# Kernel tuning notes

Measured on AMD Instinct MI355X. Metric: run time of the kernel, lower is better.

The kernel has to match this reference:

```python
import jax, jax.numpy as jnp
import numpy as np

N_LAYERS = 11
DILATIONS = tuple(2 ** i for i in range(N_LAYERS))   # 1..1024
MEM_SIZES = DILATIONS                                 # kernel=2 -> 1 past tap -> mem = dilation
HOP = 128
C_SCALE = 1.0
FFT = 256       # channel width
NUM_CLS = 256   # mu-law classes
COND = 80       # mel bands
FRAMES = 16


def setup_inputs() -> dict:
    key = jax.random.key(0)
    ks = jax.random.split(key, 10)
    s = 0.05  # keep logits well-scaled for softmax sampling
    return {
        "y": jax.random.normal(ks[0], (COND, FRAMES), jnp.float32),
        "samples": jax.random.uniform(ks[1], (FRAMES * HOP,), jnp.float32),
        "emb_raw": jax.random.normal(ks[2], (NUM_CLS, FFT), jnp.float32) * 0.5,
        "condition_W": jax.random.normal(ks[3], (N_LAYERS * FFT, COND), jnp.float32) * s,
        "WV_past": jax.random.normal(ks[4], (N_LAYERS, FFT, FFT, 1), jnp.float32) * s,
        "WV_present": jax.random.normal(ks[5], (N_LAYERS, FFT, FFT), jnp.float32) * s,
        "W_o_w": jax.random.normal(ks[6], (N_LAYERS, FFT, FFT), jnp.float32) * s,
        "W_o_b": jax.random.normal(ks[7], (N_LAYERS, FFT), jnp.float32) * s,
        "end_w": jax.random.normal(ks[8], (NUM_CLS, FFT), jnp.float32) * s,
        "end_b": jax.random.normal(ks[9], (NUM_CLS,), jnp.float32) * s,
    }


def reference(y, samples, emb_raw, condition_W, WV_past, WV_present, W_o_w, W_o_b, end_w, end_b):
    emb = jnp.tanh(emb_raw)                      # fftnet.emb[0].weight.tanh()
    T = y.shape[1] * HOP
    # F.interpolate nearest with scale_factor=hop_length == frame repeat
    yu = jnp.repeat(y, HOP, axis=1)              # [COND, T]
    # precompute all conditioning projections (condition_W @ y[:, i], chunked per layer)
    conds = (condition_W @ yu).reshape(N_LAYERS, FFT, T).transpose(2, 0, 1)  # [T, L, FFT]

    bufs0 = tuple(jnp.zeros((FFT, m), jnp.float32) for m in MEM_SIZES)
    x0 = emb[NUM_CLS // 2 - 1]
    n_taps = WV_past.shape[3]

    def step(carry, inp):
        x, bufs = carry
        cond_t, u, t = inp
        new_bufs = []
        for j in range(N_LAYERS):
            mem = bufs[j]
            m = MEM_SIZES[j]
            idx = t % m                                   # ring-buffer write/oldest-read ptr
            h = cond_t[j]
            ii = idx
            for k in range(n_taps):                       # read past taps (before write)
                h = h + WV_past[j, :, :, k] @ mem[:, ii]
                ii = (ii + DILATIONS[j]) % m
            h = h + WV_present[j] @ x
            new_bufs.append(mem.at[:, idx].set(x))        # write current x into ring buffer
            h = jax.nn.relu(h)
            z = W_o_w[j] @ h + W_o_b[j]
            x = jax.nn.relu(z + x)                        # residual + relu
        logits = (end_w @ x + end_b) * C_SCALE
        cum = jnp.cumsum(jax.nn.softmax(logits))
        new_idx = jnp.argmax(cum > u)                     # nonzero(cum > u)[0]
        return (emb[new_idx], tuple(new_bufs)), new_idx

    ts = jnp.arange(T)
    _, outputs = jax.lax.scan(step, (x0, bufs0), (conds, samples, ts))
    return outputs  # [T] int sampled mu-law classes
```

## Files before the change

kernel.cpp:

```cpp
#include <hip/hip_runtime.h>
#include <math.h>


#define T_STEPS 2048
#define NBLK    33

#define OFF_EMBT   0
#define OFF_WPET   65536
#define OFF_WVPET  131072
#define OFF_RINGS  196608
#define OFF_TAPS   1244672
#define OFF_Z      1285632
#define OFF_H0     1291264
#define WS_FLOATS  1291520

#define FZ(j,s)  ((((j)*2)+(s))*32)
#define FTAP(j)  ((21+(j))*32)
#define FH0      (32*32)
#define FBAR(b)  ((40+(b))*32)
#define NZERO_INTS  1280
#define NFLAG_INTS  4096

__device__ __forceinline__ float ldc(const float* p) {
  int v = __hip_atomic_load((const int*)p, __ATOMIC_RELAXED, __HIP_MEMORY_SCOPE_AGENT);
  return __int_as_float(v);
}
__device__ __forceinline__ void stc(float* p, float x) {
  __hip_atomic_store((int*)p, __float_as_int(x), __ATOMIC_RELAXED, __HIP_MEMORY_SCOPE_AGENT);
}
__device__ __forceinline__ void wait1(int* f, int want) {
  int it = 0;
  while (__hip_atomic_load(f, __ATOMIC_RELAXED, __HIP_MEMORY_SCOPE_AGENT) < want) {
    if (++it > (1 << 24)) break;
  }
  (void)__hip_atomic_load(f, __ATOMIC_ACQUIRE, __HIP_MEMORY_SCOPE_AGENT);
}
__device__ __forceinline__ void post(int* f, int v) {
  __hip_atomic_store(f, v, __ATOMIC_RELEASE, __HIP_MEMORY_SCOPE_AGENT);
}

__global__ __launch_bounds__(512)
void fftnet_kernel(const float* __restrict__ y, const float* __restrict__ samples,
                   const float* __restrict__ emb_raw, const float* __restrict__ condW,
                   const float* __restrict__ WV_past, const float* __restrict__ WV_present,
                   const float* __restrict__ W_o_w, const float* __restrict__ W_o_b,
                   const float* __restrict__ end_w, const float* __restrict__ end_b,
                   int* __restrict__ out, float* __restrict__ ws)
{
  const int tid = threadIdx.x;
  const int bid = blockIdx.x;
  int* iflags = (int*)(ws + WS_FLOATS);

  __shared__ float s_x[256];
  __shared__ float s_h[256];
  __shared__ float s_p[1024];
  __shared__ float s_cond[16 * 256];
  __shared__ float s_m[320];
  __shared__ unsigned long long s_mask[8];
  __shared__ int s_i[16];

  if (bid == 0) {
    for (int i = tid; i < NZERO_INTS; i += 512)
      __hip_atomic_store(iflags + i, 0, __ATOMIC_RELAXED, __HIP_MEMORY_SCOPE_AGENT);
  }
  for (int i = bid * 512 + tid; i < 65536; i += NBLK * 512)
    stc(ws + OFF_EMBT + i, tanhf(emb_raw[i]));

  __syncthreads();
  if (tid == 0) post(iflags + FBAR(bid), 1);
  if (tid < NBLK) wait1(iflags + FBAR(tid), 1);
  __syncthreads();

  for (int n = bid; n < 512; n += NBLK) {
    const float* wmat = (n < 256) ? WV_present : WV_past;
    int cls = n & 255;
    int c = tid & 255, s2 = tid >> 8;
    float acc = 0.f;
    for (int k = 128 * s2; k < 128 * s2 + 128; ++k)
      acc += wmat[c * 256 + k] * ws[OFF_EMBT + cls * 256 + k];
    s_p[s2 * 256 + c] = acc;
    __syncthreads();
    if (tid < 256)
      stc(ws + ((n < 256) ? OFF_WPET : OFF_WVPET) + cls * 256 + tid, s_p[tid] + s_p[256 + tid]);
    __syncthreads();
  }

  __syncthreads();
  if (tid == 0) post(iflags + FBAR(bid), 2);
  if (tid < NBLK) wait1(iflags + FBAR(tid), 2);
  __syncthreads();

  if (bid == 0) {
    const int c = tid & 255, s2 = tid >> 8;
    float we[128];
#pragma unroll
    for (int i = 0; i < 128; ++i) we[i] = end_w[c * 256 + 128 * s2 + i];
    const float eb = end_b[c];
    const float b10 = W_o_b[10 * 256 + c];
    for (int e = tid; e < 4096; e += 512) {
      int f = e >> 8, r = e & 255;
      float a = 0.f;
      for (int q = 0; q < 80; ++q) a += condW[r * 80 + q] * y[q * 16 + f];
      s_cond[f * 256 + r] = a;
    }
    __syncthreads();
    float* h0 = ws + OFF_H0;
    float* ring0 = ws + OFF_RINGS;
    float* zA = ws + OFF_Z + (10 * 2 + 0) * 256;
    float* zB = ws + OFF_Z + (10 * 2 + 1) * 256;
    float* ring10 = ws + OFF_RINGS + 512 * 1023;
    if (tid < 256) {
      float hv = s_cond[tid] + ws[OFF_WPET + 127 * 256 + tid];
      stc(h0 + tid, fmaxf(hv, 0.f));
      stc(ring0 + tid, ws[OFF_EMBT + 127 * 256 + tid]);
    }
    __syncthreads();
    if (tid == 0) post(iflags + FH0, 1);
    int pidx = 127;
    const int lane = tid & 63, w = tid >> 6;

    for (int t = 0; t < T_STEPS; ++t) {
      float qv = (tid < 256) ? ws[OFF_WVPET + pidx * 256 + tid] : 0.f;
      if (tid < 2) wait1(iflags + FZ(10, tid), t + 1);
      __syncthreads();
      if (tid < 256) {
        float xo = ldc(zA + tid) + ldc(zB + tid) + b10 + ldc(ring10 + (t & 2047) * 256 + tid);
        s_x[tid] = fmaxf(xo, 0.f);
      }
      __syncthreads();
      float acc = 0.f;
#pragma unroll
      for (int i = 0; i < 128; ++i) acc += we[i] * s_x[128 * s2 + i];
      s_p[s2 * 256 + c] = acc;
      __syncthreads();
      float logit = 0.f;
      if (tid < 256) logit = s_p[tid] + s_p[256 + tid] + eb;
      float vmax = (tid < 256) ? logit : -3.4e38f;
#pragma unroll
      for (int d = 32; d > 0; d >>= 1) vmax = fmaxf(vmax, __shfl_xor(vmax, d, 64));
      if (lane == 0) s_m[280 + w] = vmax;
      __syncthreads();
      float mx = fmaxf(fmaxf(s_m[280], s_m[281]), fmaxf(s_m[282], s_m[283]));
      float e = (tid < 256) ? expf(logit - mx) : 0.f;
      float vs = e;
#pragma unroll
      for (int d = 32; d > 0; d >>= 1) vs += __shfl_xor(vs, d, 64);
      if (lane == 0) s_m[288 + w] = vs;
      __syncthreads();
      float ssum = s_m[288] + s_m[289] + s_m[290] + s_m[291];
      float u = samples[t];
      float p = (tid < 256) ? (e / ssum) : 0.f;
      float v = p;
#pragma unroll
      for (int d = 1; d < 64; d <<= 1) {
        float o = __shfl_up(v, (unsigned)d, 64);
        if (lane >= d) v += o;
      }
      if (tid < 256 && lane == 63) s_m[256 + w] = v;
      __syncthreads();
      float offs = 0.f;
      if (tid < 256) for (int k = 0; k < w; ++k) offs += s_m[256 + k];
      float cum = v + offs;
      unsigned long long msk = __ballot(tid < 256 && (cum > u));
      if (lane == 0) s_mask[w] = msk;
      __syncthreads();
      if (tid == 0) {
        int idx = 0;
        for (int k = 0; k < 4; ++k) {
          unsigned long long m2 = s_mask[k];
          if (m2) { idx = k * 64 + (int)__builtin_ctzll(m2); break; }
        }
        s_i[0] = idx;
        out[t] = idx;
      }
      __syncthreads();
      int idx = s_i[0];
      if (t + 1 < T_STEPS) {
        int f1 = (t + 1) >> 7;
        if (tid < 256) {
          float hv = s_cond[f1 * 256 + tid] + ws[OFF_WPET + idx * 256 + tid] + qv;
          stc(h0 + tid, fmaxf(hv, 0.f));
          stc(ring0 + ((t + 1) & 1) * 256 + tid, ws[OFF_EMBT + idx * 256 + tid]);
        }
        __syncthreads();
        if (tid == 0) post(iflags + FH0, t + 2);
      }
      pidx = idx;
    }

  } else if (bid <= 22) {
    int j, side;
    if (bid <= 10)      { j = bid;      side = 0; }
    else if (bid <= 20) { j = bid - 10; side = 1; }
    else                { j = 0;        side = bid - 21; }
    const int base = side * 128;
    float wo[64];
    {
      const float* W = W_o_w + j * 65536;
      int c = tid & 255, s2 = tid >> 8;
#pragma unroll
      for (int i = 0; i < 64; ++i) wo[i] = W[c * 256 + base + 64 * s2 + i];
    }

    if (j == 0) {
      float* h0 = ws + OFF_H0;
      float* zout = ws + OFF_Z + side * 256;
      const int c = tid & 255, s2 = tid >> 8;
      for (int t = 0; t < T_STEPS; ++t) {
        if (tid == 0) wait1(iflags + FH0, t + 1);
        __syncthreads();
        if (tid < 128) s_h[tid] = ldc(h0 + base + tid);
        __syncthreads();
        float acc = 0.f;
#pragma unroll
        for (int i = 0; i < 64; ++i) acc += wo[i] * s_h[64 * s2 + i];
        s_p[s2 * 256 + c] = acc;
        __syncthreads();
        if (tid < 256) stc(zout + tid, s_p[tid] + s_p[256 + tid]);
        __syncthreads();
        if (tid == 0) post(iflags + FZ(0, side), t + 1);
      }
    } else {
      float wp[64];
      {
        const float* W = WV_present + j * 65536;
        int r = tid & 127, s = tid >> 7;
#pragma unroll
        for (int i = 0; i < 64; ++i) wp[i] = W[(base + r) * 256 + 64 * s + i];
      }
      const float bprev = W_o_b[(j - 1) * 256 + (tid & 255)];
      for (int e = tid; e < 2048; e += 512) {
        int f = e >> 7, rr = e & 127;
        float a = 0.f;
        for (int q = 0; q < 80; ++q) a += condW[(j * 256 + base + rr) * 80 + q] * y[q * 16 + f];
        s_cond[f * 128 + rr] = a;
      }
      __syncthreads();
      const int dj = 1 << j, maskj = 2 * dj - 1;
      const int dprev = 1 << (j - 1), maskp = 2 * dprev - 1;
      float* ringp = ws + OFF_RINGS + 512 * (dprev - 1);
      float* ringj = ws + OFF_RINGS + 512 * (dj - 1);
      float* zpa = ws + OFF_Z + ((j - 1) * 2 + 0) * 256;
      float* zpb = ws + OFF_Z + ((j - 1) * 2 + 1) * 256;
      float* zout = ws + OFF_Z + (j * 2 + side) * 256;
      float* tapj = ws + OFF_TAPS + (j - 1) * 16 * 256;

      for (int t = 0; t < T_STEPS; ++t) {
        if (tid == 0) wait1(iflags + FTAP(j), t + 1);
        __syncthreads();
        float tv = (tid < 128) ? ldc(tapj + (t & 15) * 256 + base + tid) : 0.f;
        if (tid < 2) wait1(iflags + FZ(j - 1, tid), t + 1);
        __syncthreads();
        if (tid < 256) {
          float xv = ldc(zpa + tid) + ldc(zpb + tid) + bprev
                   + ldc(ringp + (t & maskp) * 256 + tid);
          xv = fmaxf(xv, 0.f);
          s_x[tid] = xv;
          if (side == 0) stc(ringj + (t & maskj) * 256 + tid, xv);
        }
        __syncthreads();
        {
          int r = tid & 127, s = tid >> 7;
          float acc = 0.f;
#pragma unroll
          for (int i = 0; i < 64; ++i) acc += wp[i] * s_x[64 * s + i];
          s_p[s * 128 + r] = acc;
        }
        __syncthreads();
        if (tid < 128) {
          int f = t >> 7;
          float hv = s_p[tid] + s_p[128 + tid] + s_p[256 + tid] + s_p[384 + tid]
                   + s_cond[f * 128 + tid] + tv;
          s_h[tid] = fmaxf(hv, 0.f);
        }
        __syncthreads();
        {
          int cc = tid & 255, s2 = tid >> 8;
          float acc = 0.f;
#pragma unroll
          for (int i = 0; i < 64; ++i) acc += wo[i] * s_h[64 * s2 + i];
          s_p[s2 * 256 + cc] = acc;
        }
        __syncthreads();
        if (tid < 256) stc(zout + tid, s_p[tid] + s_p[256 + tid]);
        __syncthreads();
        if (tid == 0) post(iflags + FZ(j, side), t + 1);
      }
    }

  } else {
    const int j = bid - 22;
    const int dj = 1 << j, maskj = 2 * dj - 1;
    float wq[128];
    {
      const float* W = WV_past + j * 65536;
      int r = tid & 255, s2 = tid >> 8;
#pragma unroll
      for (int i = 0; i < 128; ++i) wq[i] = W[r * 256 + 128 * s2 + i];
    }
    float* ringj = ws + OFF_RINGS + 512 * (dj - 1);
    float* tapj = ws + OFF_TAPS + (j - 1) * 16 * 256;
    const int lag = (dj < 16) ? dj : 16;

    for (int t = 0; t < T_STEPS; ++t) {
      int want = t - lag + 1;
      if (tid == 0 && want >= 1) wait1(iflags + FZ(j, 0), want);
      __syncthreads();
      if (t >= dj) {
        if (tid < 256) s_x[tid] = ldc(ringj + ((t - dj) & maskj) * 256 + tid);
        __syncthreads();
        int r = tid & 255, s2 = tid >> 8;
        float acc = 0.f;
#pragma unroll
        for (int i = 0; i < 128; ++i) acc += wq[i] * s_x[128 * s2 + i];
        s_p[s2 * 256 + r] = acc;
        __syncthreads();
        if (tid < 256) stc(tapj + (t & 15) * 256 + tid, s_p[tid] + s_p[256 + tid]);
      } else {
        if (tid < 256) stc(tapj + (t & 15) * 256 + tid, 0.f);
      }
      __syncthreads();
      if (tid == 0) post(iflags + FTAP(j), t + 1);
    }
  }
}

extern "C" void kernel_launch(void* const* d_in, const int* in_sizes, int n_in,
                              void* d_out, int out_size, void* d_ws, size_t ws_size,
                              hipStream_t stream) {
  const float* y       = (const float*)d_in[0];
  const float* samples = (const float*)d_in[1];
  const float* emb_raw = (const float*)d_in[2];
  const float* condW   = (const float*)d_in[3];
  const float* WV_past = (const float*)d_in[4];
  const float* WV_pres = (const float*)d_in[5];
  const float* W_o_w   = (const float*)d_in[6];
  const float* W_o_b   = (const float*)d_in[7];
  const float* end_w   = (const float*)d_in[8];
  const float* end_b   = (const float*)d_in[9];
  (void)in_sizes; (void)n_in; (void)out_size; (void)ws_size;
  hipLaunchKernelGGL(fftnet_kernel, dim3(NBLK), dim3(512), 0, stream,
                     y, samples, emb_raw, condW, WV_past, WV_pres,
                     W_o_w, W_o_b, end_w, end_b, (int*)d_out, (float*)d_ws);
}
```

Baseline: 59.14 ms.

## Pin pipeline roles to one XCC and use L2-coherent CAS loads for handoff

```diff
diff --git a/kernel.cpp b/kernel.cpp
--- a/kernel.cpp
+++ b/kernel.cpp
@@ -3,7 +3,8 @@
 
 
 #define T_STEPS 2048
-#define NBLK    33
+#define NROLE   32
+#define NBLK    256
 
 #define OFF_EMBT   0
 #define OFF_WPET   65536
@@ -11,27 +12,25 @@
 #define OFF_RINGS  196608
 #define OFF_TAPS   1244672
 #define OFF_Z      1285632
-#define OFF_H0     1291264
 #define WS_FLOATS  1291520
 
 #define FZ(j,s)  ((((j)*2)+(s))*32)
 #define FTAP(j)  ((21+(j))*32)
-#define FH0      (32*32)
-#define FBAR(b)  ((40+(b))*32)
-#define NZERO_INTS  1280
-#define NFLAG_INTS  4096
-
-__device__ __forceinline__ float ldc(const float* p) {
-  int v = __hip_atomic_load((const int*)p, __ATOMIC_RELAXED, __HIP_MEMORY_SCOPE_AGENT);
-  return __int_as_float(v);
-}
+#define FIDX     (32*32)
+#define FBAR(r)  ((40+(r))*32)
+#define NZERO_INTS 1280
+#define CHOSEN   2432
+#define TICKET   2464
+
+#define XCC_GETREG ((31 << 11) | 20)
+
 __device__ __forceinline__ void stc(float* p, float x) {
   __hip_atomic_store((int*)p, __float_as_int(x), __ATOMIC_RELAXED, __HIP_MEMORY_SCOPE_AGENT);
 }
 __device__ __forceinline__ void wait1(int* f, int want) {
   int it = 0;
   while (__hip_atomic_load(f, __ATOMIC_RELAXED, __HIP_MEMORY_SCOPE_AGENT) < want) {
-    if (++it > (1 << 24)) break;
+    if (++it > (1 << 22)) break;
   }
   (void)__hip_atomic_load(f, __ATOMIC_ACQUIRE, __HIP_MEMORY_SCOPE_AGENT);
 }
@@ -39,7 +38,28 @@
   __hip_atomic_store(f, v, __ATOMIC_RELEASE, __HIP_MEMORY_SCOPE_AGENT);
 }
 
-__global__ __launch_bounds__(512)
+#define SENT  0x7fffffff
+#define SENT2 0x7ffffffe
+__device__ __forceinline__ int ld_i32_l2(int* p) {
+  int e = SENT;
+  __hip_atomic_compare_exchange_strong(p, &e, SENT2, __ATOMIC_RELAXED,
+                                       __ATOMIC_RELAXED, __HIP_MEMORY_SCOPE_WORKGROUP);
+  return e;
+}
+__device__ __forceinline__ float ld_f32_l2(float* p) {
+  int e = SENT;
+  __hip_atomic_compare_exchange_strong((int*)p, &e, SENT2, __ATOMIC_RELAXED,
+                                       __ATOMIC_RELAXED, __HIP_MEMORY_SCOPE_WORKGROUP);
+  return __int_as_float(e);
+}
+__device__ __forceinline__ int wait_l2(int* f, int want, int& budget) {
+  int v;
+  do { v = ld_i32_l2(f); } while (v < want && --budget > 0);
+  return v;
+}
+__device__ __forceinline__ void drain() { asm volatile("s_waitcnt vmcnt(0)" ::: "memory"); }
+
+__global__ __launch_bounds__(512, 2)
 void fftnet_kernel(const float* __restrict__ y, const float* __restrict__ samples,
                    const float* __restrict__ emb_raw, const float* __restrict__ condW,
                    const float* __restrict__ WV_past, const float* __restrict__ WV_present,
@@ -48,7 +68,6 @@
                    int* __restrict__ out, float* __restrict__ ws)
 {
   const int tid = threadIdx.x;
-  const int bid = blockIdx.x;
   int* iflags = (int*)(ws + WS_FLOATS);
 
   __shared__ float s_x[256];
@@ -57,21 +76,46 @@
   __shared__ float s_cond[16 * 256];
   __shared__ float s_m[320];
   __shared__ unsigned long long s_mask[8];
-  __shared__ int s_i[16];
-
-  if (bid == 0) {
-    for (int i = tid; i < NZERO_INTS; i += 512)
-      __hip_atomic_store(iflags + i, 0, __ATOMIC_RELAXED, __HIP_MEMORY_SCOPE_AGENT);
-  }
-  for (int i = bid * 512 + tid; i < 65536; i += NBLK * 512)
+  __shared__ int s_i[2];
+
+  if (blockIdx.x == 0) {
+    for (int i = tid; i < NZERO_INTS; i += 512) iflags[i] = 0;
+    drain();
+    if (tid == 0)
+      __hip_atomic_store(iflags + TICKET, 0, __ATOMIC_RELAXED, __HIP_MEMORY_SCOPE_AGENT);
+    __threadfence();
+    __syncthreads();
+    if (tid == 0) {
+      int xcc = __builtin_amdgcn_s_getreg(XCC_GETREG) & 15;
+      __hip_atomic_store(iflags + CHOSEN, xcc + 1, __ATOMIC_RELEASE, __HIP_MEMORY_SCOPE_AGENT);
+    }
+  }
+  if (tid == 0) {
+    int ch, it = 0;
+    do {
+      ch = __hip_atomic_load(iflags + CHOSEN, __ATOMIC_ACQUIRE, __HIP_MEMORY_SCOPE_AGENT);
+    } while ((ch < 1 || ch > 16) && ++it < (1 << 24));
+    int xcc = __builtin_amdgcn_s_getreg(XCC_GETREG) & 15;
+    int role = -1;
+    if (xcc == ch - 1) {
+      int tk = __hip_atomic_fetch_add(iflags + TICKET, 1, __ATOMIC_RELAXED,
+                                      __HIP_MEMORY_SCOPE_AGENT);
+      if (tk < NROLE) role = tk;
+    }
+    s_i[0] = role;
+  }
+  __syncthreads();
+  const int role = s_i[0];
+  if (role < 0) return;
+
+  for (int i = role * 512 + tid; i < 65536; i += NROLE * 512)
     stc(ws + OFF_EMBT + i, tanhf(emb_raw[i]));
-
-  __syncthreads();
-  if (tid == 0) post(iflags + FBAR(bid), 1);
-  if (tid < NBLK) wait1(iflags + FBAR(tid), 1);
-  __syncthreads();
-
-  for (int n = bid; n < 512; n += NBLK) {
+  __syncthreads();
+  if (tid == 0) post(iflags + FBAR(role), 1);
+  if (tid < NROLE) wait1(iflags + FBAR(tid), 1);
+  __syncthreads();
+
+  for (int n = role; n < 512; n += NROLE) {
     const float* wmat = (n < 256) ? WV_present : WV_past;
     int cls = n & 255;
     int c = tid & 255, s2 = tid >> 8;
@@ -84,48 +128,37 @@
       stc(ws + ((n < 256) ? OFF_WPET : OFF_WVPET) + cls * 256 + tid, s_p[tid] + s_p[256 + tid]);
     __syncthreads();
   }
-
-  __syncthreads();
-  if (tid == 0) post(iflags + FBAR(bid), 2);
-  if (tid < NBLK) wait1(iflags + FBAR(tid), 2);
-  __syncthreads();
-
-  if (bid == 0) {
+  __syncthreads();
+  if (tid == 0) post(iflags + FBAR(role), 2);
+  if (tid < NROLE) wait1(iflags + FBAR(tid), 2);
+  __syncthreads();
+  __builtin_amdgcn_fence(__ATOMIC_ACQUIRE, "agent");
+  __syncthreads();
+
+  int budget = 1 << 22;
+
+  if (role == 0) {
     const int c = tid & 255, s2 = tid >> 8;
     float we[128];
 #pragma unroll
     for (int i = 0; i < 128; ++i) we[i] = end_w[c * 256 + 128 * s2 + i];
     const float eb = end_b[c];
     const float b10 = W_o_b[10 * 256 + c];
-    for (int e = tid; e < 4096; e += 512) {
-      int f = e >> 8, r = e & 255;
-      float a = 0.f;
-      for (int q = 0; q < 80; ++q) a += condW[r * 80 + q] * y[q * 16 + f];
-      s_cond[f * 256 + r] = a;
-    }
-    __syncthreads();
-    float* h0 = ws + OFF_H0;
-    float* ring0 = ws + OFF_RINGS;
     float* zA = ws + OFF_Z + (10 * 2 + 0) * 256;
     float* zB = ws + OFF_Z + (10 * 2 + 1) * 256;
     float* ring10 = ws + OFF_RINGS + 512 * 1023;
-    if (tid < 256) {
-      float hv = s_cond[tid] + ws[OFF_WPET + 127 * 256 + tid];
-      stc(h0 + tid, fmaxf(hv, 0.f));
-      stc(ring0 + tid, ws[OFF_EMBT + 127 * 256 + tid]);
-    }
-    __syncthreads();
-    if (tid == 0) post(iflags + FH0, 1);
-    int pidx = 127;
     const int lane = tid & 63, w = tid >> 6;
+    if (tid == 0) iflags[FIDX] = (1 << 8) | 127;
 
     for (int t = 0; t < T_STEPS; ++t) {
-      float qv = (tid < 256) ? ws[OFF_WVPET + pidx * 256 + tid] : 0.f;
-      if (tid < 2) wait1(iflags + FZ(10, tid), t + 1);
+      float u = samples[t];
+      if (tid < 2) wait_l2(iflags + FZ(10, 0) + tid * 32, t + 1, budget);
       __syncthreads();
       if (tid < 256) {
-        float xo = ldc(zA + tid) + ldc(zB + tid) + b10 + ldc(ring10 + (t & 2047) * 256 + tid);
-        s_x[tid] = fmaxf(xo, 0.f);
+        float a = ld_f32_l2(zA + tid);
+        float b = ld_f32_l2(zB + tid);
+        float r3 = ld_f32_l2(ring10 + (t & 2047) * 256 + tid);
+        s_x[tid] = fmaxf(a + b + b10 + r3, 0.f);
       }
       __syncthreads();
       float acc = 0.f;
@@ -148,7 +181,6 @@
       if (lane == 0) s_m[288 + w] = vs;
       __syncthreads();
       float ssum = s_m[288] + s_m[289] + s_m[290] + s_m[291];
-      float u = samples[t];
       float p = (tid < 256) ? (e / ssum) : 0.f;
       float v = p;
 #pragma unroll
@@ -170,144 +202,155 @@
           unsigned long long m2 = s_mask[k];
           if (m2) { idx = k * 64 + (int)__builtin_ctzll(m2); break; }
         }
-        s_i[0] = idx;
+        iflags[FIDX] = ((t + 2) << 8) | idx;
         out[t] = idx;
       }
       __syncthreads();
-      int idx = s_i[0];
-      if (t + 1 < T_STEPS) {
-        int f1 = (t + 1) >> 7;
-        if (tid < 256) {
-          float hv = s_cond[f1 * 256 + tid] + ws[OFF_WPET + idx * 256 + tid] + qv;
-          stc(h0 + tid, fmaxf(hv, 0.f));
-          stc(ring0 + ((t + 1) & 1) * 256 + tid, ws[OFF_EMBT + idx * 256 + tid]);
+    }
+
+  } else if (role == 1) {
+    float wo0[128];
+    { int c = tid & 255, s2 = tid >> 8;
+#pragma unroll
+      for (int i = 0; i < 128; ++i) wo0[i] = W_o_w[c * 256 + 128 * s2 + i]; }
+    const float b0 = W_o_b[tid & 255];
+    for (int e = tid; e < 4096; e += 512) {
+      int f = e >> 8, r = e & 255;
+      float a = 0.f;
+      for (int q = 0; q < 80; ++q) a += condW[r * 80 + q] * y[q * 16 + f];
+      s_cond[f * 256 + r] = a;
+    }
+    __syncthreads();
+    float* x1 = ws + OFF_Z;
+    int pidx = 127;
+
+    for (int t = 0; t < T_STEPS; ++t) {
+      float tapv = 0.f;
+      if (tid < 256 && t > 0) tapv = ws[OFF_WVPET + pidx * 256 + tid];
+      if (tid == 0) {
+        int v = wait_l2(iflags + FIDX, (t + 1) << 8, budget);
+        s_i[1] = v & 255;
+      }
+      __syncthreads();
+      const int idx = s_i[1];
+      if (tid < 256) {
+        s_x[tid] = ws[OFF_EMBT + idx * 256 + tid];
+        float hv = s_cond[(t >> 7) * 256 + tid] + ws[OFF_WPET + idx * 256 + tid] + tapv;
+        s_h[tid] = fmaxf(hv, 0.f);
+      }
+      __syncthreads();
+      {
+        int c = tid & 255, s2 = tid >> 8;
+        float a0 = 0.f, a1 = 0.f;
+#pragma unroll
+        for (int i = 0; i < 64; ++i) a0 += wo0[i] * s_h[128 * s2 + i];
+#pragma unroll
+        for (int i = 0; i < 64; ++i) a1 += wo0[64 + i] * s_h[128 * s2 + 64 + i];
+        s_p[s2 * 256 + c] = a0 + a1;
+      }
+      __syncthreads();
+      if (tid < 256)
+        x1[tid] = fmaxf(s_p[tid] + s_p[256 + tid] + b0 + s_x[tid], 0.f);
+      drain();
+      __syncthreads();
+      if (tid == 0) iflags[FZ(0, 0)] = t + 1;
+      pidx = idx;
+    }
+
+  } else if (role <= 21) {
+    const int jj = (role <= 11) ? (role - 1) : (role - 11);
+    const int side = (role <= 11) ? 0 : 1;
+    const int base = side * 128;
+    float wp[64], wo[64];
+    { const float* W = WV_present + jj * 65536;
+      int r = tid & 127, s = tid >> 7;
+#pragma unroll
+      for (int i = 0; i < 64; ++i) wp[i] = W[(base + r) * 256 + 64 * s + i]; }
+    { const float* W = W_o_w + jj * 65536;
+      int c = tid & 255, s2 = tid >> 8;
+#pragma unroll
+      for (int i = 0; i < 64; ++i) wo[i] = W[c * 256 + base + 64 * s2 + i]; }
+    const float bprev = W_o_b[(jj - 1) * 256 + (tid & 255)];
+    for (int e = tid; e < 2048; e += 512) {
+      int f = e >> 7, rr = e & 127;
+      float a = 0.f;
+      for (int q = 0; q < 80; ++q) a += condW[(jj * 256 + base + rr) * 80 + q] * y[q * 16 + f];
+      s_cond[f * 128 + rr] = a;
+    }
+    __syncthreads();
+    const int dj = 1 << jj, maskj = 2 * dj - 1;
+    const int dprev = 1 << (jj - 1), maskp = 2 * dprev - 1;
+    float* ringp = ws + OFF_RINGS + 512 * (dprev - 1);
+    float* ringj = ws + OFF_RINGS + 512 * (dj - 1);
+    float* zpa = ws + OFF_Z + ((jj - 1) * 2 + 0) * 256;
+    float* zpb = ws + OFF_Z + ((jj - 1) * 2 + 1) * 256;
+    float* zout = ws + OFF_Z + (jj * 2 + side) * 256;
+    float* tapj = ws + OFF_TAPS + (jj - 1) * 16 * 256;
+    const int nz = (jj == 1) ? 1 : 2;
+
+    for (int t = 0; t < T_STEPS; ++t) {
+      if (tid < nz) wait_l2(iflags + FZ(jj - 1, 0) + tid * 32, t + 1, budget);
+      if (tid == 2) wait_l2(iflags + FTAP(jj), t + 1, budget);
+      __syncthreads();
+      float tv = 0.f;
+      if (tid < 256) {
+        float xv;
+        if (jj == 1) {
+          xv = ld_f32_l2(zpa + tid);
+        } else {
+          float a = ld_f32_l2(zpa + tid);
+          float b = ld_f32_l2(zpb + tid);
+          float r3 = ld_f32_l2(ringp + (t & maskp) * 256 + tid);
+          xv = fmaxf(a + b + bprev + r3, 0.f);
         }
-        __syncthreads();
-        if (tid == 0) post(iflags + FH0, t + 2);
-      }
-      pidx = idx;
-    }
-
-  } else if (bid <= 22) {
-    int j, side;
-    if (bid <= 10)      { j = bid;      side = 0; }
-    else if (bid <= 20) { j = bid - 10; side = 1; }
-    else                { j = 0;        side = bid - 21; }
-    const int base = side * 128;
-    float wo[64];
-    {
-      const float* W = W_o_w + j * 65536;
-      int c = tid & 255, s2 = tid >> 8;
-#pragma unroll
-      for (int i = 0; i < 64; ++i) wo[i] = W[c * 256 + base + 64 * s2 + i];
-    }
-
-    if (j == 0) {
-      float* h0 = ws + OFF_H0;
-      float* zout = ws + OFF_Z + side * 256;
-      const int c = tid & 255, s2 = tid >> 8;
-      for (int t = 0; t < T_STEPS; ++t) {
-        if (tid == 0) wait1(iflags + FH0, t + 1);
-        __syncthreads();
-        if (tid < 128) s_h[tid] = ldc(h0 + base + tid);
-        __syncthreads();
+        s_x[tid] = xv;
+        if (side == 0) ringj[(t & maskj) * 256 + tid] = xv;
+      }
+      if (tid < 128) tv = ld_f32_l2(tapj + (t & 15) * 256 + base + tid);
+      __syncthreads();
+      { int r = tid & 127, s = tid >> 7;
         float acc = 0.f;
 #pragma unroll
+        for (int i = 0; i < 64; ++i) acc += wp[i] * s_x[64 * s + i];
+        s_p[s * 128 + r] = acc; }
+      __syncthreads();
+      if (tid < 128) {
+        int f = t >> 7;
+        float hv = s_p[tid] + s_p[128 + tid] + s_p[256 + tid] + s_p[384 + tid]
+                 + s_cond[f * 128 + tid] + tv;
+        s_h[tid] = fmaxf(hv, 0.f);
+      }
+      __syncthreads();
+      { int cc = tid & 255, s2 = tid >> 8;
+        float acc = 0.f;
+#pragma unroll
         for (int i = 0; i < 64; ++i) acc += wo[i] * s_h[64 * s2 + i];
-        s_p[s2 * 256 + c] = acc;
-        __syncthreads();
-        if (tid < 256) stc(zout + tid, s_p[tid] + s_p[256 + tid]);
-        __syncthreads();
-        if (tid == 0) post(iflags + FZ(0, side), t + 1);
-      }
-    } else {
-      float wp[64];
-      {
-        const float* W = WV_present + j * 65536;
-        int r = tid & 127, s = tid >> 7;
-#pragma unroll
-        for (int i = 0; i < 64; ++i) wp[i] = W[(base + r) * 256 + 64 * s + i];
-      }
-      const float bprev = W_o_b[(j - 1) * 256 + (tid & 255)];
-      for (int e = tid; e < 2048; e += 512) {
-        int f = e >> 7, rr = e & 127;
-        float a = 0.f;
-        for (int q = 0; q < 80; ++q) a += condW[(j * 256 + base + rr) * 80 + q] * y[q * 16 + f];
-        s_cond[f * 128 + rr] = a;
-      }
-      __syncthreads();
-      const int dj = 1 << j, maskj = 2 * dj - 1;
-      const int dprev = 1 << (j - 1), maskp = 2 * dprev - 1;
-      float* ringp = ws + OFF_RINGS + 512 * (dprev - 1);
-      float* ringj = ws + OFF_RINGS + 512 * (dj - 1);
-      float* zpa = ws + OFF_Z + ((j - 1) * 2 + 0) * 256;
-      float* zpb = ws + OFF_Z + ((j - 1) * 2 + 1) * 256;
-      float* zout = ws + OFF_Z + (j * 2 + side) * 256;
-      float* tapj = ws + OFF_TAPS + (j - 1) * 16 * 256;
-
-      for (int t = 0; t < T_STEPS; ++t) {
-        if (tid == 0) wait1(iflags + FTAP(j), t + 1);
-        __syncthreads();
-        float tv = (tid < 128) ? ldc(tapj + (t & 15) * 256 + base + tid) : 0.f;
-        if (tid < 2) wait1(iflags + FZ(j - 1, tid), t + 1);
-        __syncthreads();
-        if (tid < 256) {
-          float xv = ldc(zpa + tid) + ldc(zpb + tid) + bprev
-                   + ldc(ringp + (t & maskp) * 256 + tid);
-          xv = fmaxf(xv, 0.f);
-          s_x[tid] = xv;
-          if (side == 0) stc(ringj + (t & maskj) * 256 + tid, xv);
-        }
-        __syncthreads();
-        {
-          int r = tid & 127, s = tid >> 7;
-          float acc = 0.f;
-#pragma unroll
-          for (int i = 0; i < 64; ++i) acc += wp[i] * s_x[64 * s + i];
-          s_p[s * 128 + r] = acc;
-        }
-        __syncthreads();
-        if (tid < 128) {
-          int f = t >> 7;
-          float hv = s_p[tid] + s_p[128 + tid] + s_p[256 + tid] + s_p[384 + tid]
-                   + s_cond[f * 128 + tid] + tv;
-          s_h[tid] = fmaxf(hv, 0.f);
-        }
-        __syncthreads();
-        {
-          int cc = tid & 255, s2 = tid >> 8;
-          float acc = 0.f;
-#pragma unroll
-          for (int i = 0; i < 64; ++i) acc += wo[i] * s_h[64 * s2 + i];
-          s_p[s2 * 256 + cc] = acc;
-        }
-        __syncthreads();
-        if (tid < 256) stc(zout + tid, s_p[tid] + s_p[256 + tid]);
-        __syncthreads();
-        if (tid == 0) post(iflags + FZ(j, side), t + 1);
-      }
+        s_p[s2 * 256 + cc] = acc; }
+      __syncthreads();
+      if (tid < 256) zout[tid] = s_p[tid] + s_p[256 + tid];
+      drain();
+      __syncthreads();
+      if (tid == 0) iflags[FZ(jj, side)] = t + 1;
     }
 
   } else {
-    const int j = bid - 22;
+    const int j = role - 21;
     const int dj = 1 << j, maskj = 2 * dj - 1;
     float wq[128];
-    {
-      const float* W = WV_past + j * 65536;
+    { const float* W = WV_past + j * 65536;
       int r = tid & 255, s2 = tid >> 8;
 #pragma unroll
-      for (int i = 0; i < 128; ++i) wq[i] = W[r * 256 + 128 * s2 + i];
-    }
+      for (int i = 0; i < 128; ++i) wq[i] = W[r * 256 + 128 * s2 + i]; }
     float* ringj = ws + OFF_RINGS + 512 * (dj - 1);
     float* tapj = ws + OFF_TAPS + (j - 1) * 16 * 256;
     const int lag = (dj < 16) ? dj : 16;
 
     for (int t = 0; t < T_STEPS; ++t) {
       int want = t - lag + 1;
-      if (tid == 0 && want >= 1) wait1(iflags + FZ(j, 0), want);
+      if (tid == 0 && want >= 1) wait_l2(iflags + FZ(j, 0), want, budget);
       __syncthreads();
       if (t >= dj) {
-        if (tid < 256) s_x[tid] = ldc(ringj + ((t - dj) & maskj) * 256 + tid);
+        if (tid < 256) s_x[tid] = ld_f32_l2(ringj + ((t - dj) & maskj) * 256 + tid);
         __syncthreads();
         int r = tid & 255, s2 = tid >> 8;
         float acc = 0.f;
@@ -315,12 +358,13 @@
         for (int i = 0; i < 128; ++i) acc += wq[i] * s_x[128 * s2 + i];
         s_p[s2 * 256 + r] = acc;
         __syncthreads();
-        if (tid < 256) stc(tapj + (t & 15) * 256 + tid, s_p[tid] + s_p[256 + tid]);
+        if (tid < 256) tapj[(t & 15) * 256 + tid] = s_p[tid] + s_p[256 + tid];
       } else {
-        if (tid < 256) stc(tapj + (t & 15) * 256 + tid, 0.f);
-      }
-      __syncthreads();
-      if (tid == 0) post(iflags + FTAP(j), t + 1);
+        if (tid < 256) tapj[(t & 15) * 256 + tid] = 0.f;
+      }
+      drain();
+      __syncthreads();
+      if (tid == 0) iflags[FTAP(j)] = t + 1;
     }
   }
 }
```

Result: slower. 64.29 ms (+8.7%).
